# Kernel optimization log

Hardware: AMD Instinct MI355X
Metric: run time of the kernel (lower is better)

The kernel has to match this reference:

```python
import jax, jax.numpy as jnp
import numpy as np
from jax import lax

B, C, O, K, L, W = 32, 128, 128, 3, 4096, 1
PAD, DIL = 1, 1


def _conv(x, w, b):
    # x: [B,C,H,W], w: [O,C,K,1] -> [B,O,H,W] (zeros padding, stride 1)
    y = lax.conv_general_dilated(x, w, window_strides=(1, 1),
                                 padding=[(PAD, PAD), (0, 0)],
                                 rhs_dilation=(DIL, 1),
                                 dimension_numbers=('NCHW', 'OIHW', 'NCHW'))
    return y + b[None, :, None, None]


def setup_inputs() -> dict:
    key = jax.random.key(0)
    ks = jax.random.split(key, 6)
    x = jax.random.normal(ks[0], (B, C, L, W), dtype=jnp.float32)
    # offset/modulator convs are zero-init in torch; use small random values to
    # exercise the deformable gather path (represents a trained state)
    w_off = jax.random.normal(ks[1], (2 * K, C, K, 1), dtype=jnp.float32) * 0.01
    b_off = jax.random.normal(ks[2], (2 * K,), dtype=jnp.float32) * 0.1
    w_mod = jax.random.normal(ks[3], (K, C, K, 1), dtype=jnp.float32) * 0.01
    b_mod = jax.random.normal(ks[4], (K,), dtype=jnp.float32) * 0.1
    w_reg = jax.random.normal(ks[5], (O, C, K, 1), dtype=jnp.float32) * (1.0 / np.sqrt(C * K))
    return {"x": x, "w_off": w_off, "b_off": b_off,
            "w_mod": w_mod, "b_mod": b_mod, "w_reg": w_reg}


def reference(x, w_off, b_off, w_mod, b_mod, w_reg):
    b, c, h, w = x.shape
    max_offset = max(h, w) / 4.0
    offset = jnp.clip(_conv(x, w_off, b_off), -max_offset, max_offset)  # [B,2K,H,W]
    mask = 2.0 * jax.nn.sigmoid(_conv(x, w_mod, b_mod))                 # [B,K,H,W]

    off = offset.reshape(b, K, 2, h, w)
    off_y, off_x = off[:, :, 0], off[:, :, 1]                           # [B,K,H,W]

    # sampling positions (stride=1, pad_w=0, kw=1)
    base_y = (-PAD + jnp.arange(K, dtype=jnp.float32)[:, None] * DIL
              + jnp.arange(h, dtype=jnp.float32)[None, :])              # [K,H]
    py = base_y[None, :, :, None] + off_y                               # [B,K,H,W]
    px = jnp.arange(w, dtype=jnp.float32)[None, None, None, :] + off_x  # [B,K,H,W]

    y0 = jnp.floor(py); x0 = jnp.floor(px)
    iy0 = y0.astype(jnp.int32); ix0 = x0.astype(jnp.int32)
    wy1 = py - y0; wy0 = 1.0 - wy1
    wx1 = px - x0; wx0 = 1.0 - wx1

    def gather(iy, ix):
        iyc = jnp.clip(iy, 0, h - 1)
        ixc = jnp.clip(ix, 0, w - 1)
        # per-batch gather: xb [C,H,W], idx [K,H,W] -> [C,K,H,W]
        return jax.vmap(lambda xb, yb, xb_i: xb[:, yb, xb_i])(x, iyc, ixc)

    acc = jnp.zeros((b, c, K, h, w), dtype=x.dtype)
    corners = [(iy0, ix0, wy0 * wx0), (iy0, ix0 + 1, wy0 * wx1),
               (iy0 + 1, ix0, wy1 * wx0), (iy0 + 1, ix0 + 1, wy1 * wx1)]
    for iy, ix, wgt in corners:
        valid = ((iy >= 0) & (iy < h) & (ix >= 0) & (ix < w)).astype(x.dtype)
        acc = acc + gather(iy, ix) * (wgt * valid)[:, None]  # [B,C,K,H,W]

    val = acc * mask[:, None]                                 # modulated samples
    out = jnp.einsum('bckhw,ock->bohw', val, w_reg[:, :, :, 0])
    return out
```

## Files before the change

### kernel.cpp

```cpp
#include <hip/hip_runtime.h>
#include <hip/hip_bf16.h>
#include <math.h>


typedef __attribute__((ext_vector_type(8))) short bf16x8;
typedef __attribute__((ext_vector_type(4))) float f32x4;
typedef float f32x2u __attribute__((ext_vector_type(2), aligned(4)));

#define WIN 160
#define WPAD 161

static __device__ inline unsigned short f2bf(float f) {
    __hip_bfloat16 h = __float2bfloat16(f);
    union { __hip_bfloat16 b; unsigned short u; } cv;
    cv.b = h;
    return cv.u;
}

__global__ __launch_bounds__(256) void k_wra(const float* __restrict__ w_reg,
                                             const float* __restrict__ w_off,
                                             const float* __restrict__ w_mod,
                                             unsigned short* __restrict__ WrA,
                                             float* __restrict__ wT) {
    int t = blockIdx.x * 256 + threadIdx.x;
    if (t < 8 * 12 * 64 * 8) {
        int e  = t & 7;
        int l  = (t >> 3) & 63;
        int ms = t >> 9;
        int m  = ms / 12;
        int s  = ms - m * 12;
        int o  = m * 16 + (l & 15);
        int kc = s * 32 + ((l >> 4) & 3) * 8 + e;
        int tap = kc >> 7;
        int c   = kc & 127;
        WrA[t] = f2bf(w_reg[(o * 128 + c) * 3 + tap]);
    } else if (t < 8 * 12 * 64 * 8 + 128 * 27) {
        int u = t - 8 * 12 * 64 * 8;
        int c = u / 27, r = u - c * 27;
        int ch = r / 3, tap = r - ch * 3;
        wT[c * 32 + r] = (ch < 6) ? w_off[(ch * 128 + c) * 3 + tap]
                                  : w_mod[((ch - 6) * 128 + c) * 3 + tap];
    }
}

__global__ __launch_bounds__(512) void k_prep(const float* __restrict__ x,
                                              const float* __restrict__ wT,
                                              const float* __restrict__ b_off,
                                              const float* __restrict__ b_mod,
                                              int* __restrict__ addr2,
                                              float* __restrict__ wae,
                                              float* __restrict__ wbe) {
    __shared__ float red[7 * 64 * 19];
    int t = threadIdx.x;
    int lane = t & 63;
    int wv = t >> 6;
    int b = blockIdx.y;
    int i = blockIdx.x * 128 + lane * 2;

    int c0 = __builtin_amdgcn_readfirstlane(wv) * 16;

    float acc[18];
#pragma unroll
    for (int z = 0; z < 18; ++z) acc[z] = 0.f;

    const float* xr = x + (size_t)b * 524288 + (size_t)c0 * 4096;
    const float* wbase = wT + c0 * 32;
#pragma unroll 2
    for (int c = 0; c < 16; ++c) {
        const float* row = xr + (size_t)c * 4096;
        f32x2u v = *(const f32x2u*)(row + i);
        float lm = row[max(i - 1, 0)];
        float rp = row[min(i + 2, 4095)];
        float left  = (i > 0)        ? lm : 0.f;
        float right = (i + 2 < 4096) ? rp : 0.f;
        const float* wrow = wbase + c * 32;
#pragma unroll
        for (int ch = 0; ch < 9; ++ch) {
            float w0 = wrow[ch * 3 + 0];
            float w1 = wrow[ch * 3 + 1];
            float w2 = wrow[ch * 3 + 2];
            acc[ch * 2 + 0] += left * w0 + v.x * w1 + v.y  * w2;
            acc[ch * 2 + 1] += v.x  * w0 + v.y * w1 + right * w2;
        }
    }

    if (wv > 0) {
        float* r = &red[((wv - 1) * 64 + lane) * 19];
#pragma unroll
        for (int z = 0; z < 18; ++z) r[z] = acc[z];
    }
    __syncthreads();
    if (wv != 0) return;

#pragma unroll
    for (int p = 0; p < 7; ++p) {
        const float* r = &red[(p * 64 + lane) * 19];
#pragma unroll
        for (int z = 0; z < 18; ++z) acc[z] += r[z];
    }

#pragma unroll
    for (int k = 0; k < 3; ++k) {
        int   av[2];
        float wav[2], wbv[2];
#pragma unroll
        for (int ii = 0; ii < 2; ++ii) {
            float offy = acc[(2 * k) * 2 + ii]     + b_off[2 * k];
            float offx = acc[(2 * k + 1) * 2 + ii] + b_off[2 * k + 1];
            offy = fminf(fmaxf(offy, -1024.f), 1024.f);
            offx = fminf(fmaxf(offx, -1024.f), 1024.f);
            float am = acc[(6 + k) * 2 + ii] + b_mod[k];
            float m  = 2.f / (1.f + expf(-am));

            float py = (float)(i + ii - 1 + k) + offy;
            float y0 = floorf(py);
            int   iy0 = (int)y0;
            float wy1 = py - y0, wy0 = 1.f - wy1;
            float x0f = floorf(offx);
            int   ix0 = (int)x0f;
            float wx1 = offx - x0f, wx0 = 1.f - wx1;

            float sx = (ix0 == 0) ? wx0 : ((ix0 == -1) ? wx1 : 0.f);
            float scal = m * sx;

            float wAv = (iy0 >= 0 && iy0 < 4096)  ? scal * wy0 : 0.f;
            float wBv = (iy0 >= -1 && iy0 < 4095) ? scal * wy1 : 0.f;

            int addr = min(max(iy0, 0), 4094);
            bool eq = (iy0 == addr);
            wav[ii] = eq ? wAv : (iy0 == -1   ? wBv : 0.f);
            wbv[ii] = eq ? wBv : (iy0 == 4095 ? wAv : 0.f);
            av[ii] = addr;
        }
        int j = (b * 3 + k) * 4096 + i;
        *(int2*)(addr2 + j)  = make_int2(av[0], av[1]);
        *(f32x2u*)(wae + j)  = (f32x2u){wav[0], wav[1]};
        *(f32x2u*)(wbe + j)  = (f32x2u){wbv[0], wbv[1]};
    }
}

__global__ __launch_bounds__(512) void k_fused(const unsigned short* __restrict__ WrA,
                                               const float* __restrict__ x,
                                               const int* __restrict__ addr2,
                                               const float* __restrict__ wae,
                                               const float* __restrict__ wbe,
                                               float* __restrict__ out) {
    __shared__ float win[32 * WPAD];
    __shared__ short Bl[2][8][3][512];
    int t = threadIdx.x;
    int l = t & 63;
    int w = t >> 6;
    int b  = blockIdx.y;
    int ib = blockIdx.x;
    int q = l >> 4;
    int il = l & 15;
    int i0t = ib * 128;
    int i0p = i0t + w * 16 + il;
    int wsod = i0t - 16;
    if (wsod > 4096 - WIN) wsod = 4096 - WIN;
    if (wsod < 0) wsod = 0;
    const float* xb = x + (size_t)b * 524288;
    const bf16x8* Ag = (const bf16x8*)WrA;

    int   a_[3];
    float wa_[3], wb_[3];
    bool  okw[3];
#pragma unroll
    for (int k = 0; k < 3; ++k) {
        int j = (b * 3 + k) * 4096 + i0p;
        int a = addr2[j];
        a_[k]  = a;
        wa_[k] = wae[j];
        wb_[k] = wbe[j];
        okw[k] = (bool)__all(a >= wsod && a <= wsod + WIN - 2);
    }

    f32x4 acc[8];
#pragma unroll
    for (int f = 0; f < 8; ++f) acc[f] = (f32x4){0.f, 0.f, 0.f, 0.f};

#pragma unroll
    for (int it = 0; it < 3; ++it) {
        int idx = it * 512 + t;
        if (idx < 1280) {
            int r  = idx / 40;
            int cp = idx - r * 40;
            float4 v = *(const float4*)(xb + (size_t)r * 4096 + wsod + cp * 4);
            float* dst = &win[r * WPAD + cp * 4];
            dst[0] = v.x; dst[1] = v.y; dst[2] = v.z; dst[3] = v.w;
        }
    }
    __syncthreads();

    for (int cc = 0; cc < 4; ++cc) {
        int p  = cc & 1;
        int cb = cc * 32;

        bf16x8 Areg[3];
#pragma unroll
        for (int k = 0; k < 3; ++k)
            Areg[k] = Ag[(w * 12 + k * 4 + cc) * 64 + l];

#pragma unroll
        for (int k = 0; k < 3; ++k) {
            float v[8];
            float wa = wa_[k], wb = wb_[k];
            if (okw[k]) {
                int pos = a_[k] - wsod;
#pragma unroll
                for (int e = 0; e < 8; ++e) {
                    const float* base = &win[(q * 8 + e) * WPAD + pos];
                    v[e] = wa * base[0] + wb * base[1];
                }
            } else {
                int a = a_[k];
#pragma unroll
                for (int e = 0; e < 8; ++e) {
                    const float* row = xb + (size_t)(cb + q * 8 + e) * 4096;
                    f32x2u p2 = *(const f32x2u*)(row + a);
                    v[e] = wa * p2.x + wb * p2.y;
                }
            }
            bf16x8 Bv;
#pragma unroll
            for (int e = 0; e < 8; ++e) Bv[e] = (short)f2bf(v[e]);
            *(bf16x8*)&Bl[p][w][k][l * 8] = Bv;
        }

        float4 stg[3];
        if (cc < 3) {
            const float* src = xb + (size_t)(cb + 32) * 4096;
#pragma unroll
            for (int it = 0; it < 3; ++it) {
                int idx = it * 512 + t;
                if (idx < 1280) {
                    int r  = idx / 40;
                    int cp = idx - r * 40;
                    stg[it] = *(const float4*)(src + (size_t)r * 4096 + wsod + cp * 4);
                }
            }
        }
        __syncthreads();

#pragma unroll
        for (int f = 0; f < 8; ++f) {
#pragma unroll
            for (int k = 0; k < 3; ++k) {
                bf16x8 Bv = *(const bf16x8*)&Bl[p][f][k][l * 8];
                acc[f] = __builtin_amdgcn_mfma_f32_16x16x32_bf16(Areg[k], Bv, acc[f], 0, 0, 0);
            }
        }

        if (cc < 3) {
#pragma unroll
            for (int it = 0; it < 3; ++it) {
                int idx = it * 512 + t;
                if (idx < 1280) {
                    int r  = idx / 40;
                    int cp = idx - r * 40;
                    float* dst = &win[r * WPAD + cp * 4];
                    dst[0] = stg[it].x; dst[1] = stg[it].y;
                    dst[2] = stg[it].z; dst[3] = stg[it].w;
                }
            }
            __syncthreads();
        }
    }

    int r0 = q * 4;
#pragma unroll
    for (int f = 0; f < 8; ++f) {
#pragma unroll
        for (int r = 0; r < 4; ++r) {
            int o = w * 16 + r0 + r;
            out[((size_t)(b * 128 + o)) * 4096 + i0t + f * 16 + il] = acc[f][r];
        }
    }
}

extern "C" void kernel_launch(void* const* d_in, const int* in_sizes, int n_in,
                              void* d_out, int out_size, void* d_ws, size_t ws_size,
                              hipStream_t stream) {
    const float* x     = (const float*)d_in[0];
    const float* w_off = (const float*)d_in[1];
    const float* b_off = (const float*)d_in[2];
    const float* w_mod = (const float*)d_in[3];
    const float* b_mod = (const float*)d_in[4];
    const float* w_reg = (const float*)d_in[5];
    float* out = (float*)d_out;

    char* ws = (char*)d_ws;
    unsigned short* WrA = (unsigned short*)(ws);
    float* wT    = (float*)(ws + 98304);
    int*   addr2 = (int*)  (ws + 131072);
    float* wae   = (float*)(ws + 1703936);
    float* wbe   = (float*)(ws + 3276800);

    k_wra<<<206, 256, 0, stream>>>(w_reg, w_off, w_mod, WrA, wT);
    k_prep<<<dim3(32, 32), 512, 0, stream>>>(x, wT, b_off, b_mod,
                                             addr2, wae, wbe);
    k_fused<<<dim3(32, 32), 512, 0, stream>>>(WrA, x, addr2, wae, wbe, out);
}
```

Before: 66.65 us.

## Compute offset/modulator conv with bf16 MFMA in prep kernel

```diff
diff --git a/kernel.cpp b/kernel.cpp
--- a/kernel.cpp
+++ b/kernel.cpp
@@ -21,9 +21,9 @@
                                              const float* __restrict__ w_off,
                                              const float* __restrict__ w_mod,
                                              unsigned short* __restrict__ WrA,
-                                             float* __restrict__ wT) {
+                                             unsigned short* __restrict__ WcA) {
     int t = blockIdx.x * 256 + threadIdx.x;
-    if (t < 8 * 12 * 64 * 8) {
+    if (t < 49152) {
         int e  = t & 7;
         int l  = (t >> 3) & 63;
         int ms = t >> 9;
@@ -34,108 +34,125 @@
         int tap = kc >> 7;
         int c   = kc & 127;
         WrA[t] = f2bf(w_reg[(o * 128 + c) * 3 + tap]);
-    } else if (t < 8 * 12 * 64 * 8 + 128 * 27) {
-        int u = t - 8 * 12 * 64 * 8;
-        int c = u / 27, r = u - c * 27;
-        int ch = r / 3, tap = r - ch * 3;
-        wT[c * 32 + r] = (ch < 6) ? w_off[(ch * 128 + c) * 3 + tap]
-                                  : w_mod[((ch - 6) * 128 + c) * 3 + tap];
-    }
-}
-
-__global__ __launch_bounds__(512) void k_prep(const float* __restrict__ x,
-                                              const float* __restrict__ wT,
-                                              const float* __restrict__ b_off,
-                                              const float* __restrict__ b_mod,
-                                              int* __restrict__ addr2,
-                                              float* __restrict__ wae,
-                                              float* __restrict__ wbe) {
-    __shared__ float red[7 * 64 * 19];
+    } else if (t < 49152 + 6144) {
+        int u = t - 49152;
+        int e = u & 7;
+        int l = (u >> 3) & 63;
+        int s = u >> 9;
+        int o = l & 15;
+        int c   = (s & 3) * 32 + ((l >> 4) & 3) * 8 + e;
+        int tap = s >> 2;
+        float v = 0.f;
+        if (o < 6)      v = w_off[(o * 128 + c) * 3 + tap];
+        else if (o < 9) v = w_mod[((o - 6) * 128 + c) * 3 + tap];
+        WcA[u] = f2bf(v);
+    }
+}
+
+__global__ __launch_bounds__(512) void k_prepm(const unsigned short* __restrict__ WcA,
+                                               const float* __restrict__ x,
+                                               const float* __restrict__ b_off,
+                                               const float* __restrict__ b_mod,
+                                               int* __restrict__ addr2,
+                                               float* __restrict__ wae,
+                                               float* __restrict__ wbe) {
+    __shared__ float win[32 * WPAD];
+    __shared__ float convx[9 * 132];
     int t = threadIdx.x;
-    int lane = t & 63;
-    int wv = t >> 6;
-    int b = blockIdx.y;
-    int i = blockIdx.x * 128 + lane * 2;
-
-    int c0 = __builtin_amdgcn_readfirstlane(wv) * 16;
-
-    float acc[18];
-#pragma unroll
-    for (int z = 0; z < 18; ++z) acc[z] = 0.f;
-
-    const float* xr = x + (size_t)b * 524288 + (size_t)c0 * 4096;
-    const float* wbase = wT + c0 * 32;
-#pragma unroll 2
-    for (int c = 0; c < 16; ++c) {
-        const float* row = xr + (size_t)c * 4096;
-        f32x2u v = *(const f32x2u*)(row + i);
-        float lm = row[max(i - 1, 0)];
-        float rp = row[min(i + 2, 4095)];
-        float left  = (i > 0)        ? lm : 0.f;
-        float right = (i + 2 < 4096) ? rp : 0.f;
-        const float* wrow = wbase + c * 32;
-#pragma unroll
-        for (int ch = 0; ch < 9; ++ch) {
-            float w0 = wrow[ch * 3 + 0];
-            float w1 = wrow[ch * 3 + 1];
-            float w2 = wrow[ch * 3 + 2];
-            acc[ch * 2 + 0] += left * w0 + v.x * w1 + v.y  * w2;
-            acc[ch * 2 + 1] += v.x  * w0 + v.y * w1 + right * w2;
-        }
-    }
-
-    if (wv > 0) {
-        float* r = &red[((wv - 1) * 64 + lane) * 19];
-#pragma unroll
-        for (int z = 0; z < 18; ++z) r[z] = acc[z];
+    int l = t & 63;
+    int w = t >> 6;
+    int b  = blockIdx.y;
+    int ib = blockIdx.x;
+    int q  = l >> 4;
+    int il = l & 15;
+    int i0t = ib * 128;
+    int wsod = i0t - 16;
+    if (wsod > 4096 - WIN) wsod = 4096 - WIN;
+    if (wsod < 0) wsod = 0;
+    const float* xb = x + (size_t)b * 524288;
+    const bf16x8* Ac = (const bf16x8*)WcA;
+    int gi = i0t + w * 16 + il;
+
+    f32x4 cv = (f32x4){0.f, 0.f, 0.f, 0.f};
+
+    for (int cc = 0; cc < 4; ++cc) {
+        int cb = cc * 32;
+        __syncthreads();
+#pragma unroll
+        for (int it = 0; it < 3; ++it) {
+            int idx = it * 512 + t;
+            if (idx < 1280) {
+                int r  = idx / 40;
+                int cp = idx - r * 40;
+                float4 v = *(const float4*)(xb + (size_t)(cb + r) * 4096 + wsod + cp * 4);
+                float* dst = &win[r * WPAD + cp * 4];
+                dst[0] = v.x; dst[1] = v.y; dst[2] = v.z; dst[3] = v.w;
+            }
+        }
+        __syncthreads();
+
+#pragma unroll
+        for (int tap = 0; tap < 3; ++tap) {
+            int s  = tap * 4 + cc;
+            int gk = gi + tap - 1;
+            bool ok = (gk >= 0) && (gk < 4096);
+            int pos = gk - wsod;
+            float vv[8];
+#pragma unroll
+            for (int e = 0; e < 8; ++e)
+                vv[e] = ok ? win[(q * 8 + e) * WPAD + pos] : 0.f;
+            bf16x8 Bv;
+#pragma unroll
+            for (int e = 0; e < 8; ++e) Bv[e] = (short)f2bf(vv[e]);
+            cv = __builtin_amdgcn_mfma_f32_16x16x32_bf16(Ac[s * 64 + l], Bv, cv, 0, 0, 0);
+        }
+    }
+
+    int ilocal = w * 16 + il;
+#pragma unroll
+    for (int rr = 0; rr < 4; ++rr) {
+        int ch = q * 4 + rr;
+        if (ch < 9) convx[ch * 132 + ilocal] = cv[rr];
     }
     __syncthreads();
-    if (wv != 0) return;
-
-#pragma unroll
-    for (int p = 0; p < 7; ++p) {
-        const float* r = &red[(p * 64 + lane) * 19];
-#pragma unroll
-        for (int z = 0; z < 18; ++z) acc[z] += r[z];
-    }
+
+    if (q != 0) return;
+    float c9[9];
+#pragma unroll
+    for (int z = 0; z < 9; ++z) c9[z] = convx[z * 132 + ilocal];
 
 #pragma unroll
     for (int k = 0; k < 3; ++k) {
-        int   av[2];
-        float wav[2], wbv[2];
-#pragma unroll
-        for (int ii = 0; ii < 2; ++ii) {
-            float offy = acc[(2 * k) * 2 + ii]     + b_off[2 * k];
-            float offx = acc[(2 * k + 1) * 2 + ii] + b_off[2 * k + 1];
-            offy = fminf(fmaxf(offy, -1024.f), 1024.f);
-            offx = fminf(fmaxf(offx, -1024.f), 1024.f);
-            float am = acc[(6 + k) * 2 + ii] + b_mod[k];
-            float m  = 2.f / (1.f + expf(-am));
-
-            float py = (float)(i + ii - 1 + k) + offy;
-            float y0 = floorf(py);
-            int   iy0 = (int)y0;
-            float wy1 = py - y0, wy0 = 1.f - wy1;
-            float x0f = floorf(offx);
-            int   ix0 = (int)x0f;
-            float wx1 = offx - x0f, wx0 = 1.f - wx1;
-
-            float sx = (ix0 == 0) ? wx0 : ((ix0 == -1) ? wx1 : 0.f);
-            float scal = m * sx;
-
-            float wAv = (iy0 >= 0 && iy0 < 4096)  ? scal * wy0 : 0.f;
-            float wBv = (iy0 >= -1 && iy0 < 4095) ? scal * wy1 : 0.f;
-
-            int addr = min(max(iy0, 0), 4094);
-            bool eq = (iy0 == addr);
-            wav[ii] = eq ? wAv : (iy0 == -1   ? wBv : 0.f);
-            wbv[ii] = eq ? wBv : (iy0 == 4095 ? wAv : 0.f);
-            av[ii] = addr;
-        }
-        int j = (b * 3 + k) * 4096 + i;
-        *(int2*)(addr2 + j)  = make_int2(av[0], av[1]);
-        *(f32x2u*)(wae + j)  = (f32x2u){wav[0], wav[1]};
-        *(f32x2u*)(wbe + j)  = (f32x2u){wbv[0], wbv[1]};
+        float offy = c9[2 * k]     + b_off[2 * k];
+        float offx = c9[2 * k + 1] + b_off[2 * k + 1];
+        offy = fminf(fmaxf(offy, -1024.f), 1024.f);
+        offx = fminf(fmaxf(offx, -1024.f), 1024.f);
+        float am = c9[6 + k] + b_mod[k];
+        float m  = 2.f / (1.f + expf(-am));
+
+        float py = (float)(gi - 1 + k) + offy;
+        float y0 = floorf(py);
+        int   iy0 = (int)y0;
+        float wy1 = py - y0, wy0 = 1.f - wy1;
+        float x0f = floorf(offx);
+        int   ix0 = (int)x0f;
+        float wx1 = offx - x0f, wx0 = 1.f - wx1;
+
+        float sx = (ix0 == 0) ? wx0 : ((ix0 == -1) ? wx1 : 0.f);
+        float scal = m * sx;
+
+        float wAv = (iy0 >= 0 && iy0 < 4096)  ? scal * wy0 : 0.f;
+        float wBv = (iy0 >= -1 && iy0 < 4095) ? scal * wy1 : 0.f;
+
+        int addr = min(max(iy0, 0), 4094);
+        bool eq = (iy0 == addr);
+        float wa = eq ? wAv : (iy0 == -1   ? wBv : 0.f);
+        float wb = eq ? wBv : (iy0 == 4095 ? wAv : 0.f);
+
+        int j = (b * 3 + k) * 4096 + gi;
+        addr2[j] = addr;
+        wae[j] = wa;
+        wbe[j] = wb;
     }
 }
 
@@ -146,7 +163,7 @@
                                                const float* __restrict__ wbe,
                                                float* __restrict__ out) {
     __shared__ float win[32 * WPAD];
-    __shared__ short Bl[2][8][3][512];
+    __shared__ short Bl[8][3][512];
     int t = threadIdx.x;
     int l = t & 63;
     int w = t >> 6;
@@ -193,7 +210,6 @@
     __syncthreads();
 
     for (int cc = 0; cc < 4; ++cc) {
-        int p  = cc & 1;
         int cb = cc * 32;
 
         bf16x8 Areg[3];
@@ -224,7 +240,7 @@
             bf16x8 Bv;
 #pragma unroll
             for (int e = 0; e < 8; ++e) Bv[e] = (short)f2bf(v[e]);
-            *(bf16x8*)&Bl[p][w][k][l * 8] = Bv;
+            *(bf16x8*)&Bl[w][k][l * 8] = Bv;
         }
 
         float4 stg[3];
@@ -242,14 +258,16 @@
         }
         __syncthreads();
 
+        __builtin_amdgcn_s_setprio(1);
 #pragma unroll
         for (int f = 0; f < 8; ++f) {
 #pragma unroll
             for (int k = 0; k < 3; ++k) {
-                bf16x8 Bv = *(const bf16x8*)&Bl[p][f][k][l * 8];
+                bf16x8 Bv = *(const bf16x8*)&Bl[f][k][l * 8];
                 acc[f] = __builtin_amdgcn_mfma_f32_16x16x32_bf16(Areg[k], Bv, acc[f], 0, 0, 0);
             }
         }
+        __builtin_amdgcn_s_setprio(0);
 
         if (cc < 3) {
 #pragma unroll
@@ -291,13 +309,13 @@
 
     char* ws = (char*)d_ws;
     unsigned short* WrA = (unsigned short*)(ws);
-    float* wT    = (float*)(ws + 98304);
+    unsigned short* WcA = (unsigned short*)(ws + 98304);
     int*   addr2 = (int*)  (ws + 131072);
     float* wae   = (float*)(ws + 1703936);
     float* wbe   = (float*)(ws + 3276800);
 
-    k_wra<<<206, 256, 0, stream>>>(w_reg, w_off, w_mod, WrA, wT);
-    k_prep<<<dim3(32, 32), 512, 0, stream>>>(x, wT, b_off, b_mod,
-                                             addr2, wae, wbe);
+    k_wra<<<216, 256, 0, stream>>>(w_reg, w_off, w_mod, WrA, WcA);
+    k_prepm<<<dim3(32, 32), 512, 0, stream>>>(WcA, x, b_off, b_mod,
+                                              addr2, wae, wbe);
     k_fused<<<dim3(32, 32), 512, 0, stream>>>(WrA, x, addr2, wae, wbe, out);
 }
```

Result: slower. 69.67 us (+4.5%).
